# Kernel tuning notes

Measured on AMD Instinct MI355X. Metric: run time of the kernel, lower is better.

Reference implementation:

```python
import jax, jax.numpy as jnp
import numpy as np

EPS = 1e-5
D_MODEL, D_INNER, D_STATE, DT_RANK, K = 2048, 4096, 16, 128, 4

def setup_inputs() -> dict:
    key = jax.random.key(0)
    ks = jax.random.split(key, 13)
    B = 128
    s = lambda k, shape, sc=0.02: jax.random.normal(k, shape, jnp.float32) * sc
    return {
        "hidden_states": jax.random.normal(ks[0], (B, 1, D_MODEL), jnp.float32),
        "conv_state": jax.random.normal(ks[1], (B, D_INNER, K - 1), jnp.float32),
        "ssm_state": jax.random.normal(ks[2], (B, D_INNER, D_STATE), jnp.float32),
        "norm_w": jnp.ones((D_MODEL,), jnp.float32),
        "in_proj_w": s(ks[3], (2 * D_INNER, D_MODEL)),           # no bias (HF Mamba default)
        "conv_w": s(ks[4], (D_INNER, K), 0.1),                    # depthwise conv kernel
        "conv_b": s(ks[5], (D_INNER,), 0.1),
        "x_proj_w": s(ks[6], (DT_RANK + 2 * D_STATE, D_INNER)),
        "dt_proj_w": s(ks[7], (D_INNER, DT_RANK)),
        "dt_proj_b": s(ks[8], (D_INNER,), 0.1),
        "A_log": jnp.log(jnp.broadcast_to(jnp.arange(1, D_STATE + 1, dtype=jnp.float32), (D_INNER, D_STATE))),
        "D": jnp.ones((D_INNER,), jnp.float32),
        "out_proj_w": s(ks[9], (D_MODEL, D_INNER)),               # no bias
    }

def reference(hidden_states, conv_state, ssm_state, norm_w, in_proj_w, conv_w, conv_b,
              x_proj_w, dt_proj_w, dt_proj_b, A_log, D, out_proj_w):
    x = hidden_states[:, 0, :]                                   # (B, d_model)
    # RMSNorm (pre-norm)
    normed = x * jax.lax.rsqrt(jnp.mean(x * x, axis=-1, keepdims=True) + EPS) * norm_w
    # in_proj -> gate z and conv branch xc
    xz = normed @ in_proj_w.T                                    # (B, 2*d_inner)
    xc, z = jnp.split(xz, 2, axis=-1)
    # depthwise causal conv, single-step with rolling cache
    conv_in = jnp.concatenate([conv_state, xc[:, :, None]], axis=-1)  # (B, d_inner, K)
    new_conv_state = conv_in[:, :, 1:]
    xact = jax.nn.silu(jnp.sum(conv_in * conv_w[None], axis=-1) + conv_b)  # (B, d_inner)
    # input-dependent SSM params
    proj = xact @ x_proj_w.T                                     # (B, dt_rank + 2*d_state)
    dt_raw = proj[:, :DT_RANK]
    Bmat = proj[:, DT_RANK:DT_RANK + D_STATE]                    # (B, d_state)
    Cmat = proj[:, DT_RANK + D_STATE:]                           # (B, d_state)
    dt = jax.nn.softplus(dt_raw @ dt_proj_w.T + dt_proj_b)       # (B, d_inner)
    A = -jnp.exp(A_log)                                          # (d_inner, d_state)
    dA = jnp.exp(dt[:, :, None] * A[None])                       # (B, d_inner, d_state)
    dB = dt[:, :, None] * Bmat[:, None, :]
    new_ssm_state = ssm_state * dA + dB * xact[:, :, None]
    y = jnp.sum(new_ssm_state * Cmat[:, None, :], axis=-1) + D * xact
    y = y * jax.nn.silu(z)
    out = y @ out_proj_w.T                                       # (B, d_model)
    output = out[:, None, :] + hidden_states                     # residual add
    return output, new_conv_state, new_ssm_state
```

## Files before the change

kernel.cpp:

```cpp
#include <hip/hip_runtime.h>

typedef __attribute__((ext_vector_type(8))) short bf16x8;
typedef __attribute__((ext_vector_type(4))) float f32x4;
typedef __attribute__((ext_vector_type(8))) unsigned short u16x8;
typedef __attribute__((ext_vector_type(4))) unsigned short u16x4;

#define DM 2048
#define DI 4096
#define BATCH 128

__device__ __forceinline__ unsigned short f2bf(float f) {
  union { float f; unsigned u; } v; v.f = f;
  unsigned r = v.u + 0x7FFFu + ((v.u >> 16) & 1u);
  return (unsigned short)(r >> 16);
}
__device__ __forceinline__ float bf2f(unsigned short u) {
  union { unsigned u; float f; } v; v.u = (unsigned)u << 16; return v.f;
}
__device__ __forceinline__ float sigm(float x) { return 1.f / (1.f + __expf(-x)); }

constexpr int BK = 64;
constexpr int LDT = BK + 8;

#define LDREGS(AR, ARF, BR, kb_) do {                                                     \
    int kb = (kb_);                                                                       \
    if constexpr (ABF) {                                                                  \
      _Pragma("unroll") for (int i = 0; i < BM / 32; ++i) {                               \
        int idx = tid + i * 256, r = idx >> 3, c = (idx & 7) * 8;                         \
        AR[i] = *(const u16x8*)&((const unsigned short*)Ag)[(long)(m0 + r) * lda + kb + c]; \
      }                                                                                   \
    } else {                                                                              \
      _Pragma("unroll") for (int i = 0; i < BM / 16; ++i) {                               \
        int idx = tid + i * 256, r = idx >> 4, c = (idx & 15) * 4;                        \
        ARF[i] = *(const f32x4*)&((const float*)Ag)[(long)(m0 + r) * lda + kb + c];       \
      }                                                                                   \
    }                                                                                     \
    _Pragma("unroll") for (int i = 0; i < BN / 16; ++i) {                                 \
      int idx = tid + i * 256, r = idx >> 4, c = (idx & 15) * 4;                          \
      BR[i] = *(const f32x4*)&Bg[(long)(n0 + r) * ldb + kb + c];                          \
    }                                                                                     \
  } while (0)

#define STLDS(AR, ARF, BR, buf_) do {                                                     \
    unsigned short* As_ = lds + (buf_) * BUF;                                             \
    unsigned short* Bs_ = As_ + BM * LDT;                                                 \
    if constexpr (ABF) {                                                                  \
      _Pragma("unroll") for (int i = 0; i < BM / 32; ++i) {                               \
        int idx = tid + i * 256, r = idx >> 3, c = (idx & 7) * 8;                         \
        *(u16x8*)&As_[r * LDT + c] = AR[i];                                               \
      }                                                                                   \
    } else {                                                                              \
      _Pragma("unroll") for (int i = 0; i < BM / 16; ++i) {                               \
        int idx = tid + i * 256, r = idx >> 4, c = (idx & 15) * 4;                        \
        u16x4 o; o[0] = f2bf(ARF[i][0]); o[1] = f2bf(ARF[i][1]);                          \
        o[2] = f2bf(ARF[i][2]); o[3] = f2bf(ARF[i][3]);                                   \
        *(u16x4*)&As_[r * LDT + c] = o;                                                   \
      }                                                                                   \
    }                                                                                     \
    _Pragma("unroll") for (int i = 0; i < BN / 16; ++i) {                                 \
      int idx = tid + i * 256, r = idx >> 4, c = (idx & 15) * 4;                          \
      u16x4 o; o[0] = f2bf(BR[i][0]); o[1] = f2bf(BR[i][1]);                              \
      o[2] = f2bf(BR[i][2]); o[3] = f2bf(BR[i][3]);                                       \
      *(u16x4*)&Bs_[r * LDT + c] = o;                                                     \
    }                                                                                     \
  } while (0)

#define COMPUTE(buf_) do {                                                                \
    const unsigned short* As_ = lds + (buf_) * BUF;                                       \
    const unsigned short* Bs_ = As_ + BM * LDT;                                           \
    _Pragma("unroll") for (int kk = 0; kk < BK; kk += 32) {                               \
      int kr = kk + lhi * 8;                                                              \
      bf16x8 af[MI], bfr[NF];                                                             \
      _Pragma("unroll") for (int mi = 0; mi < MI; ++mi)                                   \
        af[mi] = *(const bf16x8*)&As_[(wm * (BM / 2) + mi * 16 + llo) * LDT + kr];        \
      _Pragma("unroll") for (int ni = 0; ni < NF; ++ni)                                   \
        bfr[ni] = *(const bf16x8*)&Bs_[(wn * 16 * NF + ni * 16 + llo) * LDT + kr];        \
      _Pragma("unroll") for (int mi = 0; mi < MI; ++mi)                                   \
        _Pragma("unroll") for (int ni = 0; ni < NF; ++ni)                                 \
          acc[mi * NF + ni] = __builtin_amdgcn_mfma_f32_16x16x32_bf16(                    \
              af[mi], bfr[ni], acc[mi * NF + ni], 0, 0, 0);                               \
    }                                                                                     \
  } while (0)

template<int BM, int BN, bool ABF>
__device__ __forceinline__ void gemmMN(const void* Ag, int lda, const float* Bg, int ldb,
                                       int m0, int n0, int k0, int k1, unsigned short* lds,
                                       f32x4* acc) {
  constexpr int NF = BN / 32;
  constexpr int MI = BM / 32;
  constexpr int BUF = (BM + BN) * LDT;
  const int tid = threadIdx.x, lane = tid & 63, wave = tid >> 6;
  const int wm = wave >> 1, wn = wave & 1, llo = lane & 15, lhi = lane >> 4;

  u16x8 ar0[ABF ? BM / 32 : 1], ar1[ABF ? BM / 32 : 1];
  f32x4 arf0[ABF ? 1 : BM / 16], arf1[ABF ? 1 : BM / 16];
  f32x4 br0[BN / 16], br1[BN / 16];

  const int nt = (k1 - k0) / BK;
  LDREGS(ar0, arf0, br0, k0);
  LDREGS(ar1, arf1, br1, k0 + BK);
  STLDS(ar0, arf0, br0, 0);
  __syncthreads();
  int t = 0;
  while (true) {
    if (t + 2 < nt) LDREGS(ar0, arf0, br0, k0 + (t + 2) * BK);
    COMPUTE(0);
    if (t + 1 < nt) STLDS(ar1, arf1, br1, 1);
    __syncthreads();
    if (++t == nt) break;
    if (t + 2 < nt) LDREGS(ar1, arf1, br1, k0 + (t + 2) * BK);
    COMPUTE(1);
    if (t + 1 < nt) STLDS(ar0, arf0, br0, 0);
    __syncthreads();
    if (++t == nt) break;
  }
}

__global__ __launch_bounds__(256) void k01_prep(const float* __restrict__ hs,
                                                const float* __restrict__ nw,
                                                unsigned short* __restrict__ normed,
                                                float* __restrict__ outp,
                                                float* __restrict__ xz,
                                                float* __restrict__ proj) {
  int blk = blockIdx.x, tid = threadIdx.x;
  int t = blk * 256 + tid;
  f32x4 z = {};
  *(f32x4*)&xz[t * 4] = z;
  if (t < 65536) *(f32x4*)&outp[t * 4] = *(const f32x4*)&hs[t * 4];
  if (t < 5120) *(f32x4*)&proj[t * 4] = z;
  if (blk < 128) {
    int b = blk;
    const float* xr = hs + (long)b * DM;
    f32x4 v0 = *(const f32x4*)&xr[tid * 4];
    f32x4 v1 = *(const f32x4*)&xr[(tid + 256) * 4];
    float ss = v0[0]*v0[0] + v0[1]*v0[1] + v0[2]*v0[2] + v0[3]*v0[3]
             + v1[0]*v1[0] + v1[1]*v1[1] + v1[2]*v1[2] + v1[3]*v1[3];
    for (int off = 32; off; off >>= 1) ss += __shfl_xor(ss, off);
    __shared__ float red[4];
    if ((tid & 63) == 0) red[tid >> 6] = ss;
    __syncthreads();
    ss = red[0] + red[1] + red[2] + red[3];
    float rstd = rsqrtf(ss * (1.f / DM) + 1e-5f);
    f32x4 w0 = *(const f32x4*)&nw[tid * 4];
    f32x4 w1 = *(const f32x4*)&nw[(tid + 256) * 4];
    u16x4 o0, o1;
#pragma unroll
    for (int j = 0; j < 4; ++j) {
      o0[j] = f2bf(v0[j] * rstd * w0[j]);
      o1[j] = f2bf(v1[j] * rstd * w1[j]);
    }
    *(u16x4*)&normed[(long)b * DM + tid * 4] = o0;
    *(u16x4*)&normed[(long)b * DM + (tid + 256) * 4] = o1;
  }
}

__global__ __launch_bounds__(256) void k2_inproj(const unsigned short* __restrict__ normed,
                                                 const float* __restrict__ W,
                                                 float* __restrict__ xz) {
  __shared__ unsigned short lds[2 * (128 + 32) * LDT];
  f32x4 acc[4] = {};
  int bn = blockIdx.x, sk = blockIdx.y;
  gemmMN<128, 32, true>(normed, DM, W, DM, 0, bn * 32, sk * 512, sk * 512 + 512, lds, acc);
  int tid = threadIdx.x, lane = tid & 63, wave = tid >> 6, wm = wave >> 1, wn = wave & 1;
  int llo = lane & 15, lhi = lane >> 4;
  int n = bn * 32 + wn * 16 + llo;
#pragma unroll
  for (int mi = 0; mi < 4; ++mi)
#pragma unroll
    for (int r = 0; r < 4; ++r) {
      int b = wm * 64 + mi * 16 + lhi * 4 + r;
      atomicAdd(&xz[(long)b * 8192 + n], acc[mi][r]);
    }
}

__global__ __launch_bounds__(256) void e2_conv(const float* __restrict__ xz,
                                               const float* __restrict__ conv_state,
                                               const float* __restrict__ conv_w,
                                               const float* __restrict__ conv_b,
                                               float* __restrict__ out_ncs,
                                               float* __restrict__ xact_f,
                                               unsigned short* __restrict__ xact_b,
                                               unsigned short* __restrict__ szb) {
  int p = blockIdx.x * 256 + threadIdx.x;
  int b = p >> 12, n = p & 4095;
  float xc = xz[(long)b * 8192 + n];
  float z  = xz[(long)b * 8192 + DI + n];
  const float* cs = conv_state + (long)p * 3;
  float c0 = cs[0], c1 = cs[1], c2 = cs[2];
  f32x4 cw = *(const f32x4*)&conv_w[n * 4];
  float xs = c0 * cw[0] + c1 * cw[1] + c2 * cw[2] + xc * cw[3] + conv_b[n];
  float xa = xs * sigm(xs);
  float* ncs = out_ncs + (long)p * 3;
  ncs[0] = c1; ncs[1] = c2; ncs[2] = xc;
  xact_f[p] = xa;
  xact_b[p] = f2bf(xa);
  szb[p] = f2bf(z * sigm(z));
}

__global__ __launch_bounds__(256) void k3_xproj(const unsigned short* __restrict__ xact_b,
                                                const float* __restrict__ XW,
                                                float* __restrict__ proj) {
  __shared__ unsigned short lds[2 * (128 + 32) * LDT];
  f32x4 acc[4] = {};
  int bn = blockIdx.x, kc = blockIdx.y;
  gemmMN<128, 32, true>(xact_b, DI, XW, DI, 0, bn * 32, kc * 128, kc * 128 + 128, lds, acc);
  int tid = threadIdx.x, lane = tid & 63, wave = tid >> 6, wm = wave >> 1, wn = wave & 1;
  int llo = lane & 15, lhi = lane >> 4;
  int n = bn * 32 + wn * 16 + llo;
#pragma unroll
  for (int mi = 0; mi < 4; ++mi)
#pragma unroll
    for (int r = 0; r < 4; ++r) {
      int b = wm * 64 + mi * 16 + lhi * 4 + r;
      atomicAdd(&proj[b * 160 + n], acc[mi][r]);
    }
}

__global__ __launch_bounds__(256) void k45_dtssm(const float* __restrict__ proj,
                                                 const float* __restrict__ DW,
                                                 const float* __restrict__ dtb,
                                                 const float* __restrict__ A_log,
                                                 const float* __restrict__ Dp,
                                                 const float* __restrict__ ssm,
                                                 const float* __restrict__ xact_f,
                                                 const unsigned short* __restrict__ szb,
                                                 float* __restrict__ out_nss,
                                                 unsigned short* __restrict__ yz_b) {
  __shared__ unsigned short lds[2 * (32 + 32) * LDT];
  f32x4 acc[1] = {};
  int nb = blockIdx.x, mb = blockIdx.y;
  gemmMN<32, 32, false>(proj, 160, DW, 128, mb * 32, nb * 32, 0, 128, lds, acc);
  int tid = threadIdx.x, lane = tid & 63, wave = tid >> 6, wm = wave >> 1, wn = wave & 1;
  int llo = lane & 15, lhi = lane >> 4;
  int n = nb * 32 + wn * 16 + llo;
  float dtbn = dtb[n], Dn = Dp[n];
  f32x4 Al0 = *(const f32x4*)&A_log[n * 16];
  f32x4 Al1 = *(const f32x4*)&A_log[n * 16 + 4];
  f32x4 Al2 = *(const f32x4*)&A_log[n * 16 + 8];
  f32x4 Al3 = *(const f32x4*)&A_log[n * 16 + 12];
  float aS[16];
#pragma unroll
  for (int j = 0; j < 4; ++j) {
    aS[j] = -__expf(Al0[j]); aS[4 + j] = -__expf(Al1[j]);
    aS[8 + j] = -__expf(Al2[j]); aS[12 + j] = -__expf(Al3[j]);
  }
#pragma unroll
  for (int r = 0; r < 4; ++r) {
    int b = mb * 32 + wm * 16 + lhi * 4 + r;
    long p = (long)b * DI + n;
    float v = acc[0][r] + dtbn;
    float dtv = (v > 20.f) ? v : log1pf(__expf(v));
    float xa = xact_f[p];
    const float* Bp = proj + b * 160 + 128;
    const float* Cp = proj + b * 160 + 144;
    const float* sp = ssm + p * 16;
    float* np = out_nss + p * 16;
    float y = 0.f;
#pragma unroll
    for (int q = 0; q < 4; ++q) {
      f32x4 sv = *(const f32x4*)&sp[q * 4];
      f32x4 Bv = *(const f32x4*)&Bp[q * 4];
      f32x4 Cv = *(const f32x4*)&Cp[q * 4];
      f32x4 nv;
#pragma unroll
      for (int j = 0; j < 4; ++j) {
        float dA = __expf(dtv * aS[q * 4 + j]);
        nv[j] = sv[j] * dA + dtv * Bv[j] * xa;
        y += nv[j] * Cv[j];
      }
      *(f32x4*)&np[q * 4] = nv;
    }
    yz_b[p] = f2bf((y + Dn * xa) * bf2f(szb[p]));
  }
}

__global__ __launch_bounds__(256) void k5_outproj(const unsigned short* __restrict__ yz_b,
                                                  const float* __restrict__ OW,
                                                  float* __restrict__ outp) {
  __shared__ unsigned short lds[2 * (128 + 32) * LDT];
  f32x4 acc[4] = {};
  int bn = blockIdx.x, sk = blockIdx.y;
  gemmMN<128, 32, true>(yz_b, DI, OW, DI, 0, bn * 32, sk * 512, sk * 512 + 512, lds, acc);
  int tid = threadIdx.x, lane = tid & 63, wave = tid >> 6, wm = wave >> 1, wn = wave & 1;
  int llo = lane & 15, lhi = lane >> 4;
  int n = bn * 32 + wn * 16 + llo;
#pragma unroll
  for (int mi = 0; mi < 4; ++mi)
#pragma unroll
    for (int r = 0; r < 4; ++r) {
      int b = wm * 64 + mi * 16 + lhi * 4 + r;
      atomicAdd(&outp[(long)b * DM + n], acc[mi][r]);
    }
}

extern "C" void kernel_launch(void* const* d_in, const int* in_sizes, int n_in, void* d_out,
                              int out_size, void* d_ws, size_t ws_size, hipStream_t stream) {
  const float* hs         = (const float*)d_in[0];
  const float* conv_state = (const float*)d_in[1];
  const float* ssm        = (const float*)d_in[2];
  const float* norm_w     = (const float*)d_in[3];
  const float* in_proj_w  = (const float*)d_in[4];
  const float* conv_w     = (const float*)d_in[5];
  const float* conv_b     = (const float*)d_in[6];
  const float* x_proj_w   = (const float*)d_in[7];
  const float* dt_proj_w  = (const float*)d_in[8];
  const float* dt_proj_b  = (const float*)d_in[9];
  const float* A_log      = (const float*)d_in[10];
  const float* Dp         = (const float*)d_in[11];
  const float* out_proj_w = (const float*)d_in[12];

  float* outp    = (float*)d_out;
  float* out_ncs = outp + 262144;
  float* out_nss = outp + 262144 + 1572864;

  char* ws = (char*)d_ws;
  unsigned short* normed = (unsigned short*)(ws);
  float*          xz     = (float*)(ws + 2097152);
  unsigned short* yz_b   = (unsigned short*)(ws + 2097152);
  float*          xact_f = (float*)(ws + 6291456);
  unsigned short* xact_b = (unsigned short*)(ws + 8388608);
  unsigned short* szb    = (unsigned short*)(ws + 9437184);
  float*          proj   = (float*)(ws + 10485760);

  hipLaunchKernelGGL(k01_prep, dim3(1024), dim3(256), 0, stream, hs, norm_w, normed, outp, xz, proj);
  hipLaunchKernelGGL(k2_inproj, dim3(256, 4), dim3(256), 0, stream, normed, in_proj_w, xz);
  hipLaunchKernelGGL(e2_conv, dim3(2048), dim3(256), 0, stream, xz, conv_state, conv_w, conv_b,
                     out_ncs, xact_f, xact_b, szb);
  hipLaunchKernelGGL(k3_xproj, dim3(5, 32), dim3(256), 0, stream, xact_b, x_proj_w, proj);
  hipLaunchKernelGGL(k45_dtssm, dim3(128, 4), dim3(256), 0, stream, proj, dt_proj_w, dt_proj_b,
                     A_log, Dp, ssm, xact_f, szb, out_nss, yz_b);
  hipLaunchKernelGGL(k5_outproj, dim3(64, 8), dim3(256), 0, stream, yz_b, out_proj_w, outp);
}
```

Baseline: 79.43 us.

## Widen in_proj tile to 64 columns and use packed bf16 conversion

The in_proj GEMM tile grows from 128x32 to 128x64 output columns, which halves the grid to 128x4 blocks and doubles the accumulators per thread, so each loaded A tile is reused across more columns. Separately, fp32-to-bf16 conversion switches from software rounding to the hardware v_cvt_pk_bf16_f32 instruction, packing two values per instruction, in the GEMM LDS staging and in RMSNorm. The larger tile uses more LDS and registers and gives fewer blocks to spread across the GPU. The hardware conversion may round differently from the manual code in edge cases such as NaN.

```diff
diff --git a/kernel.cpp b/kernel.cpp
--- a/kernel.cpp
+++ b/kernel.cpp
@@ -4,6 +4,7 @@
 typedef __attribute__((ext_vector_type(4))) float f32x4;
 typedef __attribute__((ext_vector_type(8))) unsigned short u16x8;
 typedef __attribute__((ext_vector_type(4))) unsigned short u16x4;
+typedef __attribute__((ext_vector_type(2))) unsigned u32x2;
 
 #define DM 2048
 #define DI 4096
@@ -16,6 +17,11 @@
 }
 __device__ __forceinline__ float bf2f(unsigned short u) {
   union { unsigned u; float f; } v; v.u = (unsigned)u << 16; return v.f;
+}
+__device__ __forceinline__ unsigned pk2bf(float lo, float hi) {
+  unsigned r;
+  asm("v_cvt_pk_bf16_f32 %0, %1, %2" : "=v"(r) : "v"(lo), "v"(hi));
+  return r;
 }
 __device__ __forceinline__ float sigm(float x) { return 1.f / (1.f + __expf(-x)); }
 
@@ -52,16 +58,14 @@
     } else {                                                                              \
       _Pragma("unroll") for (int i = 0; i < BM / 16; ++i) {                               \
         int idx = tid + i * 256, r = idx >> 4, c = (idx & 15) * 4;                        \
-        u16x4 o; o[0] = f2bf(ARF[i][0]); o[1] = f2bf(ARF[i][1]);                          \
-        o[2] = f2bf(ARF[i][2]); o[3] = f2bf(ARF[i][3]);                                   \
-        *(u16x4*)&As_[r * LDT + c] = o;                                                   \
+        u32x2 o; o[0] = pk2bf(ARF[i][0], ARF[i][1]); o[1] = pk2bf(ARF[i][2], ARF[i][3]); \
+        *(u32x2*)&As_[r * LDT + c] = o;                                                   \
       }                                                                                   \
     }                                                                                     \
     _Pragma("unroll") for (int i = 0; i < BN / 16; ++i) {                                 \
       int idx = tid + i * 256, r = idx >> 4, c = (idx & 15) * 4;                          \
-      u16x4 o; o[0] = f2bf(BR[i][0]); o[1] = f2bf(BR[i][1]);                              \
-      o[2] = f2bf(BR[i][2]); o[3] = f2bf(BR[i][3]);                                       \
-      *(u16x4*)&Bs_[r * LDT + c] = o;                                                     \
+      u32x2 o; o[0] = pk2bf(BR[i][0], BR[i][1]); o[1] = pk2bf(BR[i][2], BR[i][3]);       \
+      *(u32x2*)&Bs_[r * LDT + c] = o;                                                     \
     }                                                                                     \
   } while (0)
 
@@ -143,34 +147,35 @@
     float rstd = rsqrtf(ss * (1.f / DM) + 1e-5f);
     f32x4 w0 = *(const f32x4*)&nw[tid * 4];
     f32x4 w1 = *(const f32x4*)&nw[(tid + 256) * 4];
-    u16x4 o0, o1;
-#pragma unroll
-    for (int j = 0; j < 4; ++j) {
-      o0[j] = f2bf(v0[j] * rstd * w0[j]);
-      o1[j] = f2bf(v1[j] * rstd * w1[j]);
-    }
-    *(u16x4*)&normed[(long)b * DM + tid * 4] = o0;
-    *(u16x4*)&normed[(long)b * DM + (tid + 256) * 4] = o1;
+    u32x2 o0, o1;
+    o0[0] = pk2bf(v0[0] * rstd * w0[0], v0[1] * rstd * w0[1]);
+    o0[1] = pk2bf(v0[2] * rstd * w0[2], v0[3] * rstd * w0[3]);
+    o1[0] = pk2bf(v1[0] * rstd * w1[0], v1[1] * rstd * w1[1]);
+    o1[1] = pk2bf(v1[2] * rstd * w1[2], v1[3] * rstd * w1[3]);
+    *(u32x2*)&normed[(long)b * DM + tid * 4] = o0;
+    *(u32x2*)&normed[(long)b * DM + (tid + 256) * 4] = o1;
   }
 }
 
 __global__ __launch_bounds__(256) void k2_inproj(const unsigned short* __restrict__ normed,
                                                  const float* __restrict__ W,
                                                  float* __restrict__ xz) {
-  __shared__ unsigned short lds[2 * (128 + 32) * LDT];
-  f32x4 acc[4] = {};
+  __shared__ unsigned short lds[2 * (128 + 64) * LDT];
+  f32x4 acc[8] = {};
   int bn = blockIdx.x, sk = blockIdx.y;
-  gemmMN<128, 32, true>(normed, DM, W, DM, 0, bn * 32, sk * 512, sk * 512 + 512, lds, acc);
+  gemmMN<128, 64, true>(normed, DM, W, DM, 0, bn * 64, sk * 512, sk * 512 + 512, lds, acc);
   int tid = threadIdx.x, lane = tid & 63, wave = tid >> 6, wm = wave >> 1, wn = wave & 1;
   int llo = lane & 15, lhi = lane >> 4;
-  int n = bn * 32 + wn * 16 + llo;
 #pragma unroll
   for (int mi = 0; mi < 4; ++mi)
 #pragma unroll
-    for (int r = 0; r < 4; ++r) {
-      int b = wm * 64 + mi * 16 + lhi * 4 + r;
-      atomicAdd(&xz[(long)b * 8192 + n], acc[mi][r]);
-    }
+    for (int ni = 0; ni < 2; ++ni)
+#pragma unroll
+      for (int r = 0; r < 4; ++r) {
+        int b = wm * 64 + mi * 16 + lhi * 4 + r;
+        int n = bn * 64 + wn * 32 + ni * 16 + llo;
+        atomicAdd(&xz[(long)b * 8192 + n], acc[mi * 2 + ni][r]);
+      }
 }
 
 __global__ __launch_bounds__(256) void e2_conv(const float* __restrict__ xz,
@@ -323,7 +328,7 @@
   float*          proj   = (float*)(ws + 10485760);
 
   hipLaunchKernelGGL(k01_prep, dim3(1024), dim3(256), 0, stream, hs, norm_w, normed, outp, xz, proj);
-  hipLaunchKernelGGL(k2_inproj, dim3(256, 4), dim3(256), 0, stream, normed, in_proj_w, xz);
+  hipLaunchKernelGGL(k2_inproj, dim3(128, 4), dim3(256), 0, stream, normed, in_proj_w, xz);
   hipLaunchKernelGGL(e2_conv, dim3(2048), dim3(256), 0, stream, xz, conv_state, conv_w, conv_b,
                      out_ncs, xact_f, xact_b, szb);
   hipLaunchKernelGGL(k3_xproj, dim3(5, 32), dim3(256), 0, stream, xact_b, x_proj_w, proj);
```

Result: faster. 77.72 us (-2.1%).
